# Performance work log

Measured on AMD Instinct MI355X. Metric: run time of the kernel, lower is better.

## Reference

```python
import jax, jax.numpy as jnp
import numpy as np

N_V, N_G, K, C_IN, DW, NB, E = 8192, 4096, 128, 128, 64, 4, 65536
SIGMA, CUT = 4.0, 8.0


def setup_inputs() -> dict:
    key = jax.random.key(0)
    ks = iter(jax.random.split(key, 64))
    s = 0.05
    def rn(shape):
        return jax.random.normal(next(ks), shape, dtype=jnp.float32) * s
    p = {}
    p['vertices'] = jax.random.uniform(next(ks), (N_V, 3), dtype=jnp.float32) * 30.0
    p['graph_pos'] = jax.random.uniform(next(ks), (N_G, 3), dtype=jnp.float32) * 30.0
    p['x_in'] = jax.random.normal(next(ks), (N_V, C_IN), dtype=jnp.float32)
    p['graph_x'] = jax.random.normal(next(ks), (N_G, C_IN), dtype=jnp.float32)
    p['mass'] = jax.random.uniform(next(ks), (N_V,), dtype=jnp.float32) + 0.5
    p['evals'] = jax.random.uniform(next(ks), (K,), dtype=jnp.float32) * 10.0
    p['evecs'] = jax.random.normal(next(ks), (N_V, K), dtype=jnp.float32) * 0.011
    p['gradX'] = jax.random.normal(next(ks), (N_V, N_V), dtype=jnp.float32) * 0.01
    p['gradY'] = jax.random.normal(next(ks), (N_V, N_V), dtype=jnp.float32) * 0.01
    p['graph_edge_index'] = jax.random.randint(next(ks), (2, E), 0, N_G)
    p['graph_edge_weight'] = jax.random.uniform(next(ks), (E,), dtype=jnp.float32)
    p['lin1_w'] = rn((C_IN, DW)); p['lin1_b'] = rn((DW,))
    p['lin2_w'] = rn((C_IN, DW)); p['lin2_b'] = rn((DW,))
    p['diff_time'] = jax.random.uniform(next(ks), (NB, DW), dtype=jnp.float32) * 0.5 + 0.01
    p['A_re'] = rn((NB, DW, DW)); p['A_im'] = rn((NB, DW, DW))
    p['mlp_w0'] = rn((NB, 3 * DW, DW)); p['mlp_b0'] = rn((NB, DW))
    p['mlp_w1'] = rn((NB, DW, DW)); p['mlp_b1'] = rn((NB, DW))
    p['mlp_w2'] = rn((NB, DW, DW)); p['mlp_b2'] = rn((NB, DW))
    p['gcn1_w'] = rn((NB, DW, DW)); p['gcn1_b'] = rn((NB, DW))
    p['gcn2_w'] = rn((NB, DW, DW)); p['gcn2_b'] = rn((NB, DW))
    p['gs_w'] = rn((NB, DW, DW)); p['gs_b'] = rn((NB, DW))
    p['sg_w'] = rn((NB, DW, DW)); p['sg_b'] = rn((NB, DW))
    return p


def _gcn_conv(x, src, dst, ew, W, b, n):
    # PyG GCNConv with self-loops (fill 1.0): D^-1/2 (A+I) D^-1/2 (x W) + b
    xw = x @ W
    deg = jnp.ones((n,), xw.dtype).at[dst].add(ew)
    dinv = 1.0 / jnp.sqrt(deg)
    norm = dinv[src] * ew * dinv[dst]
    agg = jnp.zeros_like(xw).at[dst].add(norm[:, None] * xw[src])
    return agg + xw / deg[:, None] + b


def _forward(vertices, graph_pos, x_in, graph_x, mass, evals, evecs, gradX, gradY,
             graph_edge_weight, lin1_w, lin1_b, lin2_w, lin2_b, diff_time, A_re, A_im,
             mlp_w0, mlp_b0, mlp_w1, mlp_b1, mlp_w2, mlp_b2,
             gcn1_w, gcn1_b, gcn2_w, gcn2_b, gs_w, gs_b, sg_w, sg_b, graph_edge_index):
    n_v = vertices.shape[0]
    # torch.cdist + cutoff + exp(-d/sigma), under no_grad in the original
    d = jnp.sqrt(jnp.maximum(jnp.sum((vertices[:, None, :] - graph_pos[None, :, :]) ** 2, -1), 0.0))
    Wb = jax.lax.stop_gradient(jnp.where(d < CUT, jnp.exp(-d / SIGMA), 0.0))  # [n_v, n_g]
    deg_v = 1.0 + Wb.sum(1)  # vertex in-degree incl. self-loop (graphsurf direction)
    deg_g = 1.0 + Wb.sum(0)  # graph-node in-degree incl. self-loop (surfgraph direction)
    rsv = 1.0 / jnp.sqrt(deg_v)
    rsg = 1.0 / jnp.sqrt(deg_g)
    src, dst = graph_edge_index[0], graph_edge_index[1]
    diff_x = x_in @ lin1_w + lin1_b
    gx = graph_x @ lin2_w + lin2_b
    n_g = gx.shape[0]
    for i in range(NB):
        # --- DiffusionNet block (spectral) ---
        t = jnp.maximum(diff_time[i], 1e-8)
        spec = evecs.T @ (diff_x * mass[:, None])              # [K, DW]
        xd = evecs @ (jnp.exp(-evals[:, None] * t[None, :]) * spec)
        gX = gradX @ xd                                         # real part of gradient
        gY = gradY @ xd                                         # imag part of gradient
        br = gX @ A_re[i] - gY @ A_im[i]
        bi = gY @ A_re[i] + gX @ A_im[i]
        gf = jnp.tanh(gX * br + gY * bi)                        # spatial gradient features
        h = jnp.concatenate([diff_x, xd, gf], axis=-1)
        h = jax.nn.relu(h @ mlp_w0[i] + mlp_b0[i])
        h = jax.nn.relu(h @ mlp_w1[i] + mlp_b1[i])
        diff_x = diff_x + h @ mlp_w2[i] + mlp_b2[i]
        # --- internal graph GCN (eval mode: dropout = identity) ---
        gx = jax.nn.relu(_gcn_conv(gx, src, dst, graph_edge_weight, gcn1_w[i], gcn1_b[i], n_g))
        gx = _gcn_conv(gx, src, dst, graph_edge_weight, gcn2_w[i], gcn2_b[i], n_g)
        # --- bipartite GCNConvs on concatenated nodes ---
        xall = jnp.concatenate([diff_x, gx], axis=0)
        xw = xall @ gs_w[i]   # graphsurf: graph -> surface edges
        os_v = xw[:n_v] / deg_v[:, None] + (Wb @ xw[n_v:]) * rsv[:, None] + gs_b[i]
        os_g = xw[n_v:] + gs_b[i]
        xw2 = xall @ sg_w[i]  # surfgraph: surface -> graph edges
        og_g = xw2[n_v:] / deg_g[:, None] + (Wb.T @ xw2[:n_v]) * rsg[:, None] + sg_b[i]
        og_v = xw2[:n_v] + sg_b[i]
        diff_x = 0.5 * (os_v + og_v)
        gx = 0.5 * (os_g + og_g)
    return diff_x  # [n_v, C_out]


def reference(vertices, graph_pos, x_in, graph_x, mass, evals, evecs, gradX, gradY,
              graph_edge_index, graph_edge_weight, lin1_w, lin1_b, lin2_w, lin2_b,
              diff_time, A_re, A_im, mlp_w0, mlp_b0, mlp_w1, mlp_b1, mlp_w2, mlp_b2,
              gcn1_w, gcn1_b, gcn2_w, gcn2_b, gs_w, gs_b, sg_w, sg_b):
    return _forward(vertices, graph_pos, x_in, graph_x, mass, evals, evecs, gradX, gradY,
                    graph_edge_weight, lin1_w, lin1_b, lin2_w, lin2_b, diff_time, A_re, A_im,
                    mlp_w0, mlp_b0, mlp_w1, mlp_b1, mlp_w2, mlp_b2,
                    gcn1_w, gcn1_b, gcn2_w, gcn2_b, gs_w, gs_b, sg_w, sg_b, graph_edge_index)
```

## Files before the change

### kernel.cpp

```cpp
#include <hip/hip_runtime.h>
#include <hip/hip_bf16.h>

typedef unsigned short u16;
typedef __attribute__((ext_vector_type(8))) short sh8;
typedef __attribute__((ext_vector_type(4))) float f32x4;

#define NV 8192
#define NG 4096
#define NE 65536

__device__ __forceinline__ u16 f2bf(float f) {
  __hip_bfloat16 h = __float2bfloat16(f);
  return __builtin_bit_cast(u16, h);
}

__device__ __forceinline__ void gl_lds16(const void* g, void* l) {
  __builtin_amdgcn_global_load_lds(
      (const __attribute__((address_space(1))) void*)g,
      (__attribute__((address_space(3))) void*)l, 16, 0, 0);
}

__global__ void k_fill4(float* __restrict__ deg_v, float* __restrict__ deg_g,
                        float* __restrict__ deg_e, int* __restrict__ cnt) {
  int i = blockIdx.x * 256 + threadIdx.x;
// ... 86 lines not shown

__global__ void k_edge_prep(const int* __restrict__ eidx, const float* __restrict__ ew,
                            float* __restrict__ deg_e, int* __restrict__ cnt) {
  int e = blockIdx.x * 256 + threadIdx.x;
  if (e < NE) { int d = eidx[NE + e]; atomicAdd(&deg_e[d], ew[e]); atomicAdd(&cnt[d], 1); }
}

__global__ __launch_bounds__(1024) void k_scan(const int* __restrict__ cnt,
    int* __restrict__ row_ptr, int* __restrict__ cursor) {
  __shared__ int buf0[1024], buf1[1024];
  int t = threadIdx.x;
  int b = t * 4;
  int c0 = cnt[b], c1 = cnt[b + 1], c2 = cnt[b + 2], c3 = cnt[b + 3];
  int s = c0 + c1 + c2 + c3;
  buf0[t] = s;
  __syncthreads();
  int* src = buf0; int* dst = buf1;
  for (int off = 1; off < 1024; off <<= 1) {
    int v = src[t];
    if (t >= off) v += src[t - off];
    dst[t] = v;
    __syncthreads();
    int* tmp = src; src = dst; dst = tmp;
  }
  int excl = (t == 0) ? 0 : src[t - 1];
  int r0 = excl, r1 = excl + c0, r2 = excl + c0 + c1, r3 = excl + c0 + c1 + c2;
  row_ptr[b] = r0; row_ptr[b + 1] = r1; row_ptr[b + 2] = r2; row_ptr[b + 3] = r3;
  cursor[b] = r0; cursor[b + 1] = r1; cursor[b + 2] = r2; cursor[b + 3] = r3;
  if (t == 1023) row_ptr[4096] = src[1023];
}

__global__ void k_scatter(const int* __restrict__ eidx, const float* __restrict__ ew,
                          const float* __restrict__ dinv, int* __restrict__ cursor,
                          int* __restrict__ csrc, float* __restrict__ cnorm) {
  int e = blockIdx.x * 256 + threadIdx.x;
  if (e < NE) {
    int s = eidx[e], d = eidx[NE + e];
    int slot = atomicAdd(&cursor[d], 1);
    csrc[slot] = s;
    cnorm[slot] = dinv[s] * ew[e] * dinv[d];
  }
}

__global__ __launch_bounds__(256) void k_evecsT(const float* __restrict__ ev, u16* __restrict__ evT) {
  __shared__ float tile[32][33];
  int t = threadIdx.x;
  int v0 = blockIdx.x * 32, k0 = blockIdx.y * 32;
  int r = t >> 3, c4 = (t & 7) * 4;
  float4 x = *(const float4*)(ev + (size_t)(v0 + r) * 128 + k0 + c4);
  tile[r][c4] = x.x; tile[r][c4 + 1] = x.y; tile[r][c4 + 2] = x.z; tile[r][c4 + 3] = x.w;
  __syncthreads();
  u16* dst = evT + (size_t)(k0 + r) * NV + v0 + c4;
  dst[0] = f2bf(tile[c4][r]); dst[1] = f2bf(tile[c4 + 1][r]);
  dst[2] = f2bf(tile[c4 + 2][r]); dst[3] = f2bf(tile[c4 + 3][r]);
}

__global__ __launch_bounds__(256) void gemm_setup3(
    const float* __restrict__ gXm, const float* __restrict__ gYm,
    const u16* __restrict__ evT, float* __restrict__ parts,
    int z, int kchunk) {
  extern __shared__ __align__(16) char smem[];
  const int t = threadIdx.x;
  const int lane = t & 63, wave = t >> 6;
  const int rl = lane & 15, hi = lane >> 4;
  int b = blockIdx.x;
  const int zi = b % z; b /= z;
  const int mb = b & 31;
  const int mat = b >> 5;
  const float* A = mat ? gYm : gXm;
  const int m0 = mb * 256;
  const int kbeg = zi * kchunk;
  const int nt = kchunk >> 5;
  const int wm = wave * 64;

  f32x4 acc[4][8];
  #pragma unroll
  for (int a = 0; a < 4; a++)
    #pragma unroll
    for (int bb = 0; bb < 8; bb++) acc[a][bb] = f32x4{0.f, 0.f, 0.f, 0.f};

  auto STAGE = [&](int buf, int k0) {
    char* aB = smem + buf * 40960;
    #pragma unroll
    for (int jj = 0; jj < 8; jj++) {
      int R0 = wave * 64 + jj * 8;
      int r = R0 + (lane >> 3);
      int s = lane & 7;
      gl_lds16(A + (size_t)(m0 + r) * NV + k0 + ((s ^ (r & 7)) << 2), aB + R0 * 128);
    }
    char* bB = smem + buf * 40960 + 32768;
    #pragma unroll
    for (int jj = 0; jj < 2; jj++) {
      int R0 = wave * 32 + jj * 16;
      int n = R0 + (lane >> 2);
      int s = lane & 3;
      gl_lds16(evT + (size_t)n * NV + k0 + ((s ^ ((n >> 1) & 3)) << 3), bB + R0 * 64);
    }
  };

  auto COMPUTE = [&](int buf) {
    const float* Af = (const float*)(smem + buf * 40960);
    const u16* Bf = (const u16*)(smem + buf * 40960 + 32768);
    sh8 av[4], bv[8];
    #pragma unroll
    for (int mf = 0; mf < 4; mf++) {
      int r = wm + mf * 16 + rl;
      f32x4 lo = *(const f32x4*)(Af + r * 32 + (((2 * hi) ^ (r & 7)) << 2));
      f32x4 h4 = *(const f32x4*)(Af + r * 32 + (((2 * hi + 1) ^ (r & 7)) << 2));
      sh8 v;
      v[0] = (short)f2bf(lo[0]); v[1] = (short)f2bf(lo[1]);
      v[2] = (short)f2bf(lo[2]); v[3] = (short)f2bf(lo[3]);
      v[4] = (short)f2bf(h4[0]); v[5] = (short)f2bf(h4[1]);
      v[6] = (short)f2bf(h4[2]); v[7] = (short)f2bf(h4[3]);
      av[mf] = v;
    }
    #pragma unroll
    for (int nf = 0; nf < 8; nf++) {
      int n = nf * 16 + rl;
      bv[nf] = *(const sh8*)(Bf + n * 32 + ((hi ^ ((n >> 1) & 3)) << 3));
    }
    #pragma unroll
    for (int mf = 0; mf < 4; mf++)
      #pragma unroll
      for (int nf = 0; nf < 8; nf++)
        acc[mf][nf] = __builtin_amdgcn_mfma_f32_16x16x32_bf16(av[mf], bv[nf], acc[mf][nf], 0, 0, 0);
  };

  STAGE(0, kbeg);
  if (nt > 1) STAGE(1, kbeg + 32);
  for (int ti = 0; ti < nt; ti++) {
    if (ti + 1 < nt) { asm volatile("s_waitcnt vmcnt(10)" ::: "memory"); }
    else             { asm volatile("s_waitcnt vmcnt(0)" ::: "memory"); }
    __builtin_amdgcn_sched_barrier(0);
    __builtin_amdgcn_s_barrier();
    COMPUTE(ti & 1);
    __builtin_amdgcn_sched_barrier(0);
    __builtin_amdgcn_s_barrier();
    if (ti + 2 < nt) STAGE(ti & 1, kbeg + (ti + 2) * 32);
  }

  float* C = parts + (size_t)(mat * z + zi) * (NV * 128);
  #pragma unroll
  for (int mf = 0; mf < 4; mf++)
    #pragma unroll
    for (int nf = 0; nf < 8; nf++) {
      int row = m0 + wm + mf * 16 + hi * 4;
      int col = nf * 16 + rl;
      #pragma unroll
      for (int q = 0; q < 4; q++)
        C[(size_t)(row + q) * 128 + col] = acc[mf][nf][q];
    }
}

__global__ __launch_bounds__(256) void gemm_panel2(
    const u16* __restrict__ WbP, const u16* __restrict__ WbTP,
    const u16* __restrict__ xwgT, const u16* __restrict__ xw2vT,
    float* __restrict__ parts) {
  __shared__ __align__(16) char smem[49152];
  const int t = threadIdx.x;
  const int lane = t & 63, wave = t >> 6;
  const int rl = lane & 15, hi = lane >> 4;
  int bid = blockIdx.x;
  const u16* Apan; const u16* BT; int KT, ldbt, mb, z;
  float* Cbase;
  if (bid < 512) {
    Apan = WbP; BT = xwgT; KT = 64; ldbt = NG;
    mb = bid >> 3; z = bid & 7;
    Cbase = parts + (size_t)z * NV * 64;
  } else {
    bid -= 512;
    Apan = WbTP; BT = xw2vT; KT = 128; ldbt = NV;
    mb = bid >> 4; z = bid & 15;
    Cbase = parts + (size_t)8 * NV * 64 + (size_t)z * NG * 64;
  }
  const int ktpz = 8;
  const int kt0 = z * ktpz;
  const int wm = wave * 32;

  f32x4 acc[2][4];
  #pragma unroll
  for (int a = 0; a < 2; a++)
    #pragma unroll
    for (int b = 0; b < 4; b++) acc[a][b] = f32x4{0.f, 0.f, 0.f, 0.f};

  auto STAGE = [&](int buf, int kt) {
    char* aB = smem + buf * 24576;
    const u16* tbase = Apan + ((size_t)mb * KT + kt) * 8192;
    #pragma unroll
    for (int jj = 0; jj < 4; jj++) {
      int j = wave * 4 + jj;
      gl_lds16(tbase + j * 512 + lane * 8, aB + j * 1024);
    }
    char* bB = aB + 16384;
    #pragma unroll
    for (int jj = 0; jj < 2; jj++) {
      int j = wave * 2 + jj;
      int n = 8 * j + (lane >> 3);
      const u16* srcb = BT + (size_t)n * ldbt + kt * 64 + (((lane & 7) ^ (n & 7)) << 3);
      gl_lds16(srcb, bB + j * 1024);
    }
  };

  auto COMPUTE = [&](int buf) {
    const u16* Af = (const u16*)(smem + buf * 24576);
    const u16* Bf = Af + 8192;
    #pragma unroll
    for (int step = 0; step < 2; step++) {
      sh8 av[2], bv[4];
      int s = step * 4 + hi;
      #pragma unroll
      for (int mf = 0; mf < 2; mf++) {
        int r = wm + mf * 16 + rl;
        av[mf] = *(const sh8*)(Af + r * 64 + ((s ^ (r & 7)) << 3));
      }
      #pragma unroll
      for (int nf = 0; nf < 4; nf++) {
        int n = nf * 16 + rl;
        bv[nf] = *(const sh8*)(Bf + n * 64 + ((s ^ (n & 7)) << 3));
      }
      #pragma unroll
      for (int mf = 0; mf < 2; mf++)
        #pragma unroll
        for (int nf = 0; nf < 4; nf++)
          acc[mf][nf] = __builtin_amdgcn_mfma_f32_16x16x32_bf16(av[mf], bv[nf], acc[mf][nf], 0, 0, 0);
    }
  };

  STAGE(0, kt0);
  STAGE(1, kt0 + 1);
  for (int ti = 0; ti < ktpz; ti++) {
    if (ti + 1 < ktpz) { asm volatile("s_waitcnt vmcnt(6)" ::: "memory"); }
    else               { asm volatile("s_waitcnt vmcnt(0)" ::: "memory"); }
    __builtin_amdgcn_sched_barrier(0);
    __builtin_amdgcn_s_barrier();
    COMPUTE(ti & 1);
    __builtin_amdgcn_sched_barrier(0);
    __builtin_amdgcn_s_barrier();
    if (ti + 2 < ktpz) STAGE(ti & 1, kt0 + ti + 2);
  }

  #pragma unroll
  for (int mf = 0; mf < 2; mf++)
    #pragma unroll
    for (int nf = 0; nf < 4; nf++) {
      int row = mb * 128 + wm + mf * 16 + hi * 4;
      int col = nf * 16 + rl;
      #pragma unroll
      for (int q = 0; q < 4; q++)
        Cbase[(size_t)(row + q) * 64 + col] = acc[mf][nf][q];
    }
}

__global__ void k_reduce_combine(const float* __restrict__ parts,
    const float* __restrict__ xw_v, const float* __restrict__ xw2_v,
    const float* __restrict__ xw_g, const float* __restrict__ xw2_g,
    const float* __restrict__ inv_deg_v, const float* __restrict__ rsv,
    const float* __restrict__ inv_deg_g, const float* __restrict__ rsg,
    const float* __restrict__ gsb, const float* __restrict__ sgb,
    float* __restrict__ dx, float* __restrict__ gx) {
  int idx = blockIdx.x * 256 + threadIdx.x;
  if (idx < NV * 64) {
    float s = parts[idx];
    #pragma unroll
    for (int z = 1; z < 8; z++) s += parts[(size_t)z * NV * 64 + idx];
    int v = idx >> 6, c = idx & 63;
    dx[idx] = 0.5f * (xw_v[idx] * inv_deg_v[v] + s * rsv[v] + gsb[c] + xw2_v[idx] + sgb[c]);
  } else {
    int j = idx - NV * 64;
    const float* src = parts + (size_t)8 * NV * 64;
    float s = src[j];
    #pragma unroll
    for (int z = 1; z < 16; z++) s += src[(size_t)z * NG * 64 + j];
    int g = j >> 6, c = j & 63;
    gx[j] = 0.5f * (xw_g[j] + gsb[c] + xw2_g[j] * inv_deg_g[g] + s * rsg[g] + sgb[c]);
  }
}

__global__ __launch_bounds__(256) void gemm_bf16(
    const u16* __restrict__ Ab, int lda, const u16* __restrict__ BT, int ldbt,
    float* __restrict__ parts, int M, int kchunk) {
  __shared__ __align__(16) char smem[49152];
  const int t = threadIdx.x;
  const int lane = t & 63, wave = t >> 6;
  const int m0 = blockIdx.x * 128;
  const int kbeg = blockIdx.z * kchunk;
  const int nt = kchunk >> 6;
  const int wm = (wave >> 1) * 64, wn = (wave & 1) * 32;
  const int arl = lane >> 3, asl = lane & 7;

  f32x4 acc[4][2];
  #pragma unroll
  for (int a = 0; a < 4; a++)
    #pragma unroll
    for (int b = 0; b < 2; b++) acc[a][b] = f32x4{0.f, 0.f, 0.f, 0.f};

  auto STAGE = [&](int buf, int k0) {
    char* base = smem + buf * 24576;
    #pragma unroll
    for (int j = 0; j < 4; j++) {
      int R0 = (wave * 4 + j) * 8;
      int r = R0 + arl;
      int gs = asl ^ (r & 7);
      gl_lds16(Ab + (size_t)(m0 + r) * lda + k0 + gs * 8, base + R0 * 128);
    }
    char* bb = base + 16384;
    #pragma unroll
    for (int j = 0; j < 2; j++) {
      int R0 = (wave * 2 + j) * 8;
      int r = R0 + arl;
      int gs = asl ^ (r & 7);
      gl_lds16(BT + (size_t)r * ldbt + k0 + gs * 8, bb + R0 * 128);
    }
  };

  auto COMPUTE = [&](int buf) {
    char* base = smem + buf * 24576;
    const u16* Af = (const u16*)base;
    const u16* Bf = (const u16*)(base + 16384);
    #pragma unroll
    for (int kk = 0; kk < 2; kk++) {
      sh8 av[4], bv[2];
      #pragma unroll
      for (int mf = 0; mf < 4; mf++) {
        int r = wm + mf * 16 + (lane & 15);
        int g = kk * 4 + (lane >> 4);
        av[mf] = *(const sh8*)(Af + r * 64 + (g ^ (r & 7)) * 8);
      }
      #pragma unroll
      for (int nf = 0; nf < 2; nf++) {
        int r = wn + nf * 16 + (lane & 15);
        int g = kk * 4 + (lane >> 4);
        bv[nf] = *(const sh8*)(Bf + r * 64 + (g ^ (r & 7)) * 8);
      }
      #pragma unroll
      for (int mf = 0; mf < 4; mf++)
        #pragma unroll
        for (int nf = 0; nf < 2; nf++)
          acc[mf][nf] = __builtin_amdgcn_mfma_f32_16x16x32_bf16(av[mf], bv[nf], acc[mf][nf], 0, 0, 0);
    }
  };

  STAGE(0, kbeg);
  if (nt > 1) STAGE(1, kbeg + 64);
  for (int ti = 0; ti < nt; ti++) {
    if (ti + 1 < nt) { asm volatile("s_waitcnt vmcnt(6)" ::: "memory"); }
    else             { asm volatile("s_waitcnt vmcnt(0)" ::: "memory"); }
    __builtin_amdgcn_sched_barrier(0);
    __builtin_amdgcn_s_barrier();
    COMPUTE(ti & 1);
    __builtin_amdgcn_sched_barrier(0);
    __builtin_amdgcn_s_barrier();
// ... 168 lines not shown
    }
  } else {
    float* lW = (float*)shm;
    int rb = bid - 128;
    for (int i = t; i < 4096; i += 256) lW[i] = W[i];
    __syncthreads();
    int row = rb * 4 + (t >> 6), c = t & 63;
    const float* Ar = gxb + (size_t)row * 64;
    float acc = 0.f;
    #pragma unroll 8
    for (int k = 0; k < 64; k++) acc += Ar[k] * lW[k * 64 + c];
    xw1[(size_t)row * 64 + c] = acc;
  }
}

__global__ __launch_bounds__(256) void k_specagg(
    const u16* __restrict__ evT, const u16* __restrict__ mdxT,
    float* __restrict__ parts,
    const float* __restrict__ xw, const int* __restrict__ rp,
    const int* __restrict__ csrc, const float* __restrict__ cnorm,
    const float* __restrict__ invdeg, const float* __restrict__ b1,
    const float* __restrict__ W2, float* __restrict__ out) {
  __shared__ __align__(16) char smem[49152];
  const int t = threadIdx.x;
  if (blockIdx.x < 64) {
    const int lane = t & 63, wave = t >> 6;
    const int kbeg = blockIdx.x * 128;
    const int wm = (wave >> 1) * 64, wn = (wave & 1) * 32;
    const int arl = lane >> 3, asl = lane & 7;
    f32x4 acc[4][2];
    #pragma unroll
    for (int a = 0; a < 4; a++)
      #pragma unroll
      for (int b = 0; b < 2; b++) acc[a][b] = f32x4{0.f, 0.f, 0.f, 0.f};
    auto STAGE = [&](int buf, int k0) {
      char* base = smem + buf * 24576;
      #pragma unroll
      for (int j = 0; j < 4; j++) {
        int R0 = (wave * 4 + j) * 8;
        int r = R0 + arl;
        int gs = asl ^ (r & 7);
        gl_lds16(evT + (size_t)r * NV + k0 + gs * 8, base + R0 * 128);
      }
      char* bb = base + 16384;
      #pragma unroll
      for (int j = 0; j < 2; j++) {
        int R0 = (wave * 2 + j) * 8;
        int r = R0 + arl;
        int gs = asl ^ (r & 7);
        gl_lds16(mdxT + (size_t)r * NV + k0 + gs * 8, bb + R0 * 128);
      }
    };
    auto COMPUTE = [&](int buf) {
      char* base = smem + buf * 24576;
      const u16* Af = (const u16*)base;
      const u16* Bf = (const u16*)(base + 16384);
      #pragma unroll
      for (int kk = 0; kk < 2; kk++) {
        sh8 av[4], bv[2];
        #pragma unroll
        for (int mf = 0; mf < 4; mf++) {
          int r = wm + mf * 16 + (lane & 15);
          int g = kk * 4 + (lane >> 4);
          av[mf] = *(const sh8*)(Af + r * 64 + (g ^ (r & 7)) * 8);
        }
        #pragma unroll
        for (int nf = 0; nf < 2; nf++) {
          int r = wn + nf * 16 + (lane & 15);
          int g = kk * 4 + (lane >> 4);
          bv[nf] = *(const sh8*)(Bf + r * 64 + (g ^ (r & 7)) * 8);
        }
        #pragma unroll
        for (int mf = 0; mf < 4; mf++)
          #pragma unroll
          for (int nf = 0; nf < 2; nf++)
            acc[mf][nf] = __builtin_amdgcn_mfma_f32_16x16x32_bf16(av[mf], bv[nf], acc[mf][nf], 0, 0, 0);
      }
    };
    STAGE(0, kbeg);
    STAGE(1, kbeg + 64);
    for (int ti = 0; ti < 2; ti++) {
      if (ti == 0) { asm volatile("s_waitcnt vmcnt(6)" ::: "memory"); }
      else         { asm volatile("s_waitcnt vmcnt(0)" ::: "memory"); }
      __builtin_amdgcn_sched_barrier(0);
      __builtin_amdgcn_s_barrier();
      COMPUTE(ti);
      __builtin_amdgcn_sched_barrier(0);
      __builtin_amdgcn_s_barrier();
    }
    float* C = parts + (size_t)blockIdx.x * 8192;
    const int lane2 = t & 63;
    #pragma unroll
    for (int mf = 0; mf < 4; mf++)
      #pragma unroll
      for (int nf = 0; nf < 2; nf++) {
        int row = wm + mf * 16 + (lane2 >> 4) * 4;
        int col = wn + nf * 16 + (lane2 & 15);
        #pragma unroll
        for (int q = 0; q < 4; q++)
          C[(size_t)(row + q) * 64 + col] = acc[mf][nf][q];
      }
  } else {
    float* lrow = (float*)smem;
    int g = (blockIdx.x - 64) * 4 + (t >> 6), c = t & 63;
    float acc = xw[(size_t)g * 64 + c] * invdeg[g] + b1[c];
    int j1 = rp[g + 1];
    for (int j = rp[g]; j < j1; j++) acc += cnorm[j] * xw[(size_t)csrc[j] * 64 + c];
    acc = fmaxf(acc, 0.f);
    lrow[t] = acc;
    __syncthreads();
    int grp = t & 192;
    float o = 0.f;
    #pragma unroll 8
    for (int k = 0; k < 64; k++) o += lrow[grp + k] * W2[k * 64 + c];
    out[(size_t)g * 64 + c] = o;
  }
}

__global__ __launch_bounds__(256) void k_redagg(
    const float* __restrict__ parts, const float* __restrict__ evals,
    const float* __restrict__ dt, float* __restrict__ Es,
    const float* __restrict__ xw, const int* __restrict__ rp,
    const int* __restrict__ csrc, const float* __restrict__ cnorm,
    const float* __restrict__ invdeg, const float* __restrict__ b2,
    const float* __restrict__ gsw, const float* __restrict__ sgw,
    float* __restrict__ xw_g, float* __restrict__ xw2_g, u16* __restrict__ xwgT) {
  __shared__ float lrow[256];
  int t = threadIdx.x;
  if (blockIdx.x < 32) {
    int i = blockIdx.x * 256 + t;
    float s = 0.f;
    #pragma unroll 8
    for (int z = 0; z < 64; z++) s += parts[(size_t)z * 8192 + i];
    int k = i >> 6, c = i & 63;
    Es[i] = expf(-evals[k] * fmaxf(dt[c], 1e-8f)) * s;
  } else {
    int g = (blockIdx.x - 32) * 4 + (t >> 6), c = t & 63;
    float acc = xw[(size_t)g * 64 + c] * invdeg[g] + b2[c];
    int j1 = rp[g + 1];
    for (int j = rp[g]; j < j1; j++) acc += cnorm[j] * xw[(size_t)csrc[j] * 64 + c];
    lrow[t] = acc;
    __syncthreads();
    int grp = t & 192;
    float p = 0.f, q = 0.f;
    #pragma unroll 8
    for (int k = 0; k < 64; k++) {
      float r = lrow[grp + k];
      p += r * gsw[k * 64 + c];
      q += r * sgw[k * 64 + c];
    }
    xw_g[(size_t)g * 64 + c] = p;
    xw2_g[(size_t)g * 64 + c] = q;
    xwgT[(size_t)c * NG + g] = f2bf(p);
  }
}

__global__ __launch_bounds__(256) void k_xdgf(const float* __restrict__ evecs,
    const float* __restrict__ GXE, const float* __restrict__ GYE,
    const float* __restrict__ Es, const float* __restrict__ Are,
    const float* __restrict__ Aim, float* __restrict__ xd, float* __restrict__ gf) {
  __shared__ float lE[8192];
  __shared__ float lr[4096], li[4096];
  __shared__ float lgx[256], lgy[256];
  int t = threadIdx.x;
  for (int i = t; i < 8192; i += 256) lE[i] = Es[i];
  for (int i = t; i < 4096; i += 256) { lr[i] = Are[i]; li[i] = Aim[i]; }
  __syncthreads();
  int wr = t >> 6, c = t & 63;
  #pragma unroll
  for (int rg = 0; rg < 2; rg++) {
    int row = blockIdx.x * 8 + rg * 4 + wr;
    const float* er = evecs + (size_t)row * 128;
    const float* xr = GXE + (size_t)row * 128;
    const float* yr = GYE + (size_t)row * 128;
    float a0 = 0, a1 = 0, a2 = 0;
    #pragma unroll 8
    for (int k = 0; k < 128; k++) {
      float s = lE[k * 64 + c];
      a0 += er[k] * s; a1 += xr[k] * s; a2 += yr[k] * s;
    }
    lgx[wr * 64 + c] = a1;
    lgy[wr * 64 + c] = a2;
    __syncthreads();
    float br = 0.f, bi = 0.f;
    #pragma unroll 8
    for (int k = 0; k < 64; k++) {
      float gx = lgx[wr * 64 + k], gy = lgy[wr * 64 + k];
      float ar = lr[k * 64 + c], ai = li[k * 64 + c];
      br += gx * ar - gy * ai;
      bi += gy * ar + gx * ai;
    }
    xd[(size_t)row * 64 + c] = a0;
    gf[(size_t)row * 64 + c] = tanhf(a1 * br + a2 * bi);
    __syncthreads();
  }
}

__global__ __launch_bounds__(256) void k_mlp0(const float* __restrict__ dx,
    const float* __restrict__ xd, const float* __restrict__ gf,
    const float* __restrict__ W0, const float* __restrict__ b0, float* __restrict__ h1) {
  __shared__ float lW[12288];
  __shared__ float lb[64];
  int t = threadIdx.x;
  for (int i = t; i < 12288; i += 256) lW[i] = W0[i];
  if (t < 64) lb[t] = b0[t];
  __syncthreads();
  int wr = t >> 6, c = t & 63;
  #pragma unroll
  for (int rg = 0; rg < 2; rg++) {
    int row = blockIdx.x * 8 + rg * 4 + wr;
    const float* a0 = dx + (size_t)row * 64;
    const float* a1 = xd + (size_t)row * 64;
    const float* a2 = gf + (size_t)row * 64;
    float acc = lb[c];
    #pragma unroll 8
    for (int k = 0; k < 64; k++) acc += a0[k] * lW[k * 64 + c];
    #pragma unroll 8
    for (int k = 0; k < 64; k++) acc += a1[k] * lW[(64 + k) * 64 + c];
    #pragma unroll 8
    for (int k = 0; k < 64; k++) acc += a2[k] * lW[(128 + k) * 64 + c];
    h1[(size_t)row * 64 + c] = fmaxf(acc, 0.f);
  }
}

__global__ __launch_bounds__(256) void k_mlp12_dual(const float* __restrict__ h1,
    const float* __restrict__ W1, const float* __restrict__ b1,
    const float* __restrict__ W2, const float* __restrict__ b2,
    const float* __restrict__ dx, const float* __restrict__ gsw,
    const float* __restrict__ sgw, float* __restrict__ xw_v,
    float* __restrict__ xw2_v, u16* __restrict__ xw2vT) {
  __shared__ float l1[4096], l2[4096], lg[4096], ls[4096];
  __shared__ float lb1[64], lb2[64], lrow[256], lrow2[256];
  int t = threadIdx.x;
  for (int i = t; i < 4096; i += 256) {
    l1[i] = W1[i]; l2[i] = W2[i]; lg[i] = gsw[i]; ls[i] = sgw[i];
  }
  if (t < 64) lb1[t] = b1[t];
  else if (t < 128) lb2[t - 64] = b2[t - 64];
  __syncthreads();
  int wr = t >> 6, c = t & 63;
  #pragma unroll
  for (int rg = 0; rg < 2; rg++) {
    int row = blockIdx.x * 8 + rg * 4 + wr;
    const float* hr = h1 + (size_t)row * 64;
    float h2 = lb1[c];
    #pragma unroll 8
    for (int k = 0; k < 64; k++) h2 += hr[k] * l1[k * 64 + c];
    h2 = fmaxf(h2, 0.f);
    lrow[wr * 64 + c] = h2;
    __syncthreads();
    float o = lb2[c] + dx[(size_t)row * 64 + c];
    #pragma unroll 8
    for (int k = 0; k < 64; k++) o += lrow[wr * 64 + k] * l2[k * 64 + c];
    lrow2[wr * 64 + c] = o;
    __syncthreads();
    float p = 0.f, q = 0.f;
    #pragma unroll 8
    for (int k = 0; k < 64; k++) {
      float a = lrow2[wr * 64 + k];
      p += a * lg[k * 64 + c];
      q += a * ls[k * 64 + c];
    }
    xw_v[(size_t)row * 64 + c] = p;
    xw2_v[(size_t)row * 64 + c] = q;
    xw2vT[(size_t)c * NV + row] = f2bf(q);
    __syncthreads();
  }
}

__global__ void k_combine(const float* __restrict__ xw_v, const float* __restrict__ Wbp,
    const float* __restrict__ xw2_v, const float* __restrict__ xw_g,
    const float* __restrict__ WbTp, const float* __restrict__ xw2_g,
    const float* __restrict__ inv_deg_v, const float* __restrict__ rsv,
    const float* __restrict__ inv_deg_g, const float* __restrict__ rsg,
    const float* __restrict__ gsb, const float* __restrict__ sgb,
    float* __restrict__ dx, float* __restrict__ gx) {
  int idx = blockIdx.x * 256 + threadIdx.x;
  if (idx < NV * 64) {
    int v = idx >> 6, c = idx & 63;
    dx[idx] = 0.5f * (xw_v[idx] * inv_deg_v[v] + Wbp[idx] * rsv[v] + gsb[c] + xw2_v[idx] + sgb[c]);
  } else {
    int j = idx - NV * 64;
    int g = j >> 6, c = j & 63;
    gx[j] = 0.5f * (xw_g[j] + gsb[c] + xw2_g[j] * inv_deg_g[g] + WbTp[j] * rsg[g] + sgb[c]);
  }
}

extern "C" void kernel_launch(void* const* d_in, const int* in_sizes, int n_in,
                              void* d_out, int out_size, void* d_ws, size_t ws_size,
                              hipStream_t stream) {
  const float* vertices  = (const float*)d_in[0];
  const float* graph_pos = (const float*)d_in[1];
  const float* x_in      = (const float*)d_in[2];
  const float* graph_x   = (const float*)d_in[3];
  const float* mass      = (const float*)d_in[4];
  const float* evals     = (const float*)d_in[5];
  const float* evecs     = (const float*)d_in[6];
  const float* gradX     = (const float*)d_in[7];
  const float* gradY     = (const float*)d_in[8];
  const int*   eidx      = (const int*)d_in[9];
  const float* ew        = (const float*)d_in[10];
  const float* lin1_w    = (const float*)d_in[11];
  const float* lin1_b    = (const float*)d_in[12];
  const float* lin2_w    = (const float*)d_in[13];
  const float* lin2_b    = (const float*)d_in[14];
  const float* diff_time = (const float*)d_in[15];
  const float* A_re      = (const float*)d_in[16];
  const float* A_im      = (const float*)d_in[17];
  const float* mlp_w0    = (const float*)d_in[18];
  const float* mlp_b0    = (const float*)d_in[19];
  const float* mlp_w1    = (const float*)d_in[20];
  const float* mlp_b1    = (const float*)d_in[21];
  const float* mlp_w2    = (const float*)d_in[22];
  const float* mlp_b2    = (const float*)d_in[23];
  const float* gcn1_w    = (const float*)d_in[24];
  const float* gcn1_b    = (const float*)d_in[25];
  const float* gcn2_w    = (const float*)d_in[26];
  const float* gcn2_b    = (const float*)d_in[27];
  const float* gs_w      = (const float*)d_in[28];
  const float* gs_b      = (const float*)d_in[29];
  const float* sg_w      = (const float*)d_in[30];
  const float* sg_b      = (const float*)d_in[31];

  char* base = (char*)d_ws;
  size_t off = 0;
  auto alloc = [&](size_t nbytes) -> void* {
    void* p = base + off;
    off += (nbytes + 255) & ~(size_t)255;
    return p;
  };
  const size_t MBy = 1024 * 1024;
  u16*   evecsT  = (u16*)alloc((size_t)128 * NV * 2);
  float* GXE2    = (float*)alloc((size_t)2 * NV * 128 * 4);
  float* GXE     = GXE2;
  float* GYE     = GXE2 + (size_t)NV * 128;
  u16*   mdxT    = (u16*)alloc((size_t)64 * NV * 2);
  float* Es      = (float*)alloc(8192 * 4);
  float* diffx   = (float*)alloc((size_t)NV * 64 * 4);
  float* gxb     = (float*)alloc((size_t)NG * 64 * 4);
  float* xd      = (float*)alloc((size_t)NV * 64 * 4);
  float* gf      = (float*)alloc((size_t)NV * 64 * 4);
  float* h1      = (float*)alloc((size_t)NV * 64 * 4);
  float* xw_v    = (float*)alloc((size_t)NV * 64 * 4);
  float* xw2_v   = (float*)alloc((size_t)NV * 64 * 4);
  float* xw_g    = (float*)alloc((size_t)NG * 64 * 4);
  float* xw2_g   = (float*)alloc((size_t)NG * 64 * 4);
  float* xw1     = (float*)alloc((size_t)NG * 64 * 4);
  float* xw2k    = (float*)alloc((size_t)NG * 64 * 4);
  u16*   xwgT    = (u16*)alloc((size_t)64 * NG * 2);
  u16*   xw2vT   = (u16*)alloc((size_t)64 * NV * 2);
  float* Wbp     = (float*)alloc((size_t)NV * 64 * 4);
  float* WbTp    = (float*)alloc((size_t)NG * 64 * 4);
  float* deg_v   = (float*)alloc(NV * 4);
  float* inv_deg_v = (float*)alloc(NV * 4);
  float* rsv     = (float*)alloc(NV * 4);
  float* deg_g   = (float*)alloc(NG * 4);
  float* inv_deg_g = (float*)alloc(NG * 4);
  float* rsg     = (float*)alloc(NG * 4);
  float* deg_e   = (float*)alloc(NG * 4);
  float* invdeg_e = (float*)alloc(NG * 4);
  float* dinv_e  = (float*)alloc(NG * 4);
  int*   cnt     = (int*)alloc(NG * 4);
  int*   row_ptr = (int*)alloc((NG + 1) * 4);
  int*   cursor  = (int*)alloc(NG * 4);
  int*   csr_src = (int*)alloc(NE * 4);
  float* csr_norm = (float*)alloc(NE * 4);

  size_t avail = ws_size > off ? ws_size - off : 0;
  u16 *WbP = nullptr, *WbTP = nullptr, *WbRow = nullptr;
  float* parts;
  int zsu;
  if (avail >= 162 * MBy) {
    WbP  = (u16*)alloc((size_t)NV * NG * 2);
    WbTP = (u16*)alloc((size_t)NG * NV * 2);
    parts = (float*)alloc(32 * MBy);
    zsu = 4;
  } else if (avail >= 97 * MBy) {
    WbRow = (u16*)alloc((size_t)NV * NG * 2);
    parts = (float*)alloc(32 * MBy);
    zsu = 4;
  } else {
    WbRow = (u16*)alloc((size_t)NV * NG * 2);
    parts = (float*)alloc(16 * MBy);
    zsu = 2;
  }
  if (off > ws_size) return;

  dim3 B256(256);

  k_fill4<<<dim3(80), B256, 0, stream>>>(deg_v, deg_g, deg_e, cnt);
  k_wb_build<<<dim3(128, 64), B256, 0, stream>>>(vertices, graph_pos, WbRow, WbP, WbTP, deg_v, deg_g);
  k_edge_prep<<<dim3(256), B256, 0, stream>>>(eidx, ew, deg_e, cnt);
  k_recips<<<dim3(64), B256, 0, stream>>>(deg_v, inv_deg_v, rsv, deg_g, inv_deg_g, rsg,
                                          deg_e, invdeg_e, dinv_e);
  k_scan<<<dim3(1), dim3(1024), 0, stream>>>(cnt, row_ptr, cursor);
  k_scatter<<<dim3(256), B256, 0, stream>>>(eidx, ew, dinv_e, cursor, csr_src, csr_norm);
  k_evecsT<<<dim3(256, 4), B256, 0, stream>>>(evecs, evecsT);
  gemm_setup3<<<dim3(2 * 32 * zsu), B256, 81920, stream>>>(
      gradX, gradY, evecsT, parts, zsu, 8192 / zsu);
  k_reduce2<<<dim3(2048), B256, 0, stream>>>(parts, GXE2, NV * 128, zsu);
  k_lin_both<<<dim3(3072), B256, 0, stream>>>(x_in, graph_x, lin1_w, lin1_b, lin2_w, lin2_b, diffx, gxb);

  for (int i = 0; i < 4; i++) {
    const float* dtrow = diff_time + i * 64;
    k_front<<<dim3(128 + 1024), B256, 0, stream>>>(diffx, mass, mdxT, gxb,
        gcn1_w + i * 4096, xw1);
    k_specagg<<<dim3(64 + 1024), B256, 0, stream>>>(evecsT, mdxT, parts,
        xw1, row_ptr, csr_src, csr_norm, invdeg_e, gcn1_b + i * 64,
        gcn2_w + i * 4096, xw2k);
    k_redagg<<<dim3(32 + 1024), B256, 0, stream>>>(parts, evals, dtrow, Es,
        xw2k, row_ptr, csr_src, csr_norm, invdeg_e, gcn2_b + i * 64,
        gs_w + i * 4096, sg_w + i * 4096, xw_g, xw2_g, xwgT);
    k_xdgf<<<dim3(1024), B256, 0, stream>>>(evecs, GXE, GYE, Es, A_re + i * 4096, A_im + i * 4096, xd, gf);
    k_mlp0<<<dim3(1024), B256, 0, stream>>>(diffx, xd, gf, mlp_w0 + i * 12288, mlp_b0 + i * 64, h1);
    k_mlp12_dual<<<dim3(1024), B256, 0, stream>>>(h1, mlp_w1 + i * 4096, mlp_b1 + i * 64,
        mlp_w2 + i * 4096, mlp_b2 + i * 64, diffx, gs_w + i * 4096, sg_w + i * 4096,
        xw_v, xw2_v, xw2vT);
    if (WbP != nullptr) {
      gemm_panel2<<<dim3(1024), B256, 0, stream>>>(WbP, WbTP, xwgT, xw2vT, parts);
      k_reduce_combine<<<dim3(3072), B256, 0, stream>>>(parts, xw_v, xw2_v, xw_g, xw2_g,
          inv_deg_v, rsv, inv_deg_g, rsg, gs_b + i * 64, sg_b + i * 64, diffx, gxb);
    } else {
      gemm_bf16<<<dim3(64, 1, 8), B256, 0, stream>>>(WbRow, NG, xwgT, NG, parts, NV, 512);
      k_reduce<<<dim3(512), B256, 0, stream>>>(parts, Wbp, NV * 64, 8);
      gemm_k<64, false, true><<<dim3(32, 1, 16), B256, 0, stream>>>(
          WbRow, nullptr, 1 << 30, xw2vT, parts, NG, 64, NG, NV, 512);
      k_reduce<<<dim3(256), B256, 0, stream>>>(parts, WbTp, NG * 64, 16);
      k_combine<<<dim3(3072), B256, 0, stream>>>(xw_v, Wbp, xw2_v, xw_g, WbTp, xw2_g,
          inv_deg_v, rsv, inv_deg_g, rsg, gs_b + i * 64, sg_b + i * 64, diffx, gxb);
    }
  }

  hipMemcpyAsync(d_out, diffx, (size_t)NV * 64 * 4, hipMemcpyDeviceToDevice, stream);
}
```

Baseline: 925.7 us.

## Overlap Wb panel GEMM with xdgf by merging into one launch

Splits the combined Wb/WbT panel GEMM. The Wb @ xw_g half depends only on the graph branch, so it now runs as extra blocks inside the xdgf kernel launch, while the WbT half runs after the MLP kernels as its own kernel. This lets the memory-heavy panel GEMM share the GPU with the VALU-bound xdgf work and moves part of the panel work off the critical path. The merged kernel uses a larger 66KB shared-memory footprint for all blocks, which may reduce occupancy of the xdgf blocks.

Result: no change. 934.1 us (+0.9%).

```diff
diff --git a/kernel.cpp b/kernel.cpp
--- a/kernel.cpp
+++ b/kernel.cpp
@@ -262,27 +262,150 @@
     }
 }
 
-__global__ __launch_bounds__(256) void gemm_panel2(
-    const u16* __restrict__ WbP, const u16* __restrict__ WbTP,
-    const u16* __restrict__ xwgT, const u16* __restrict__ xw2vT,
+__global__ __launch_bounds__(256) void k_xdgf_wbp(
+    const float* __restrict__ evecs, const float* __restrict__ GXE,
+    const float* __restrict__ GYE, const float* __restrict__ Es,
+    const float* __restrict__ Are, const float* __restrict__ Aim,
+    float* __restrict__ xd, float* __restrict__ gf,
+    const u16* __restrict__ WbP, const u16* __restrict__ xwgT,
+    float* __restrict__ parts) {
+  __shared__ __align__(16) char shm[67584];
+  const int t = threadIdx.x;
+  if (blockIdx.x < 1024) {
+    float* lE  = (float*)shm;
+    float* lr  = lE + 8192;
+    float* li  = lr + 4096;
+    float* lgx = li + 4096;
+    float* lgy = lgx + 256;
+    for (int i = t; i < 8192; i += 256) lE[i] = Es[i];
+    for (int i = t; i < 4096; i += 256) { lr[i] = Are[i]; li[i] = Aim[i]; }
+    __syncthreads();
+    int wr = t >> 6, c = t & 63;
+    #pragma unroll
+    for (int rg = 0; rg < 2; rg++) {
+      int row = blockIdx.x * 8 + rg * 4 + wr;
+      const float* er = evecs + (size_t)row * 128;
+      const float* xr = GXE + (size_t)row * 128;
+      const float* yr = GYE + (size_t)row * 128;
+      float a0 = 0, a1 = 0, a2 = 0;
+      #pragma unroll 8
+      for (int k = 0; k < 128; k++) {
+        float s = lE[k * 64 + c];
+        a0 += er[k] * s; a1 += xr[k] * s; a2 += yr[k] * s;
+      }
+      lgx[wr * 64 + c] = a1;
+      lgy[wr * 64 + c] = a2;
+      __syncthreads();
+      float br = 0.f, bi = 0.f;
+      #pragma unroll 8
+      for (int k = 0; k < 64; k++) {
+        float gx = lgx[wr * 64 + k], gy = lgy[wr * 64 + k];
+        float ar = lr[k * 64 + c], ai = li[k * 64 + c];
+        br += gx * ar - gy * ai;
+        bi += gy * ar + gx * ai;
+      }
+      xd[(size_t)row * 64 + c] = a0;
+      gf[(size_t)row * 64 + c] = tanhf(a1 * br + a2 * bi);
+      __syncthreads();
+    }
+  } else {
+    char* smem = shm;
+    const int lane = t & 63, wave = t >> 6;
+    const int rl = lane & 15, hi = lane >> 4;
+    int bid = blockIdx.x - 1024;
+    const int mb = bid >> 3, z = bid & 7;
+    const int KT = 64;
+    float* Cbase = parts + (size_t)z * NV * 64;
+    const int ktpz = 8;
+    const int kt0 = z * ktpz;
+    const int wm = wave * 32;
+
+    f32x4 acc[2][4];
+    #pragma unroll
+    for (int a = 0; a < 2; a++)
+      #pragma unroll
+      for (int b = 0; b < 4; b++) acc[a][b] = f32x4{0.f, 0.f, 0.f, 0.f};
+
+    auto STAGE = [&](int buf, int kt) {
+      char* aB = smem + buf * 24576;
+      const u16* tbase = WbP + ((size_t)mb * KT + kt) * 8192;
+      #pragma unroll
+      for (int jj = 0; jj < 4; jj++) {
+        int j = wave * 4 + jj;
+        gl_lds16(tbase + j * 512 + lane * 8, aB + j * 1024);
+      }
+      char* bB = aB + 16384;
+      #pragma unroll
+      for (int jj = 0; jj < 2; jj++) {
+        int j = wave * 2 + jj;
+        int n = 8 * j + (lane >> 3);
+        const u16* srcb = xwgT + (size_t)n * NG + kt * 64 + (((lane & 7) ^ (n & 7)) << 3);
+        gl_lds16(srcb, bB + j * 1024);
+      }
+    };
+
+    auto COMPUTE = [&](int buf) {
+      const u16* Af = (const u16*)(smem + buf * 24576);
+      const u16* Bf = Af + 8192;
+      #pragma unroll
+      for (int step = 0; step < 2; step++) {
+        sh8 av[2], bv[4];
+        int s = step * 4 + hi;
+        #pragma unroll
+        for (int mf = 0; mf < 2; mf++) {
+          int r = wm + mf * 16 + rl;
+          av[mf] = *(const sh8*)(Af + r * 64 + ((s ^ (r & 7)) << 3));
+        }
+        #pragma unroll
+        for (int nf = 0; nf < 4; nf++) {
+          int n = nf * 16 + rl;
+          bv[nf] = *(const sh8*)(Bf + n * 64 + ((s ^ (n & 7)) << 3));
+        }
+        #pragma unroll
+        for (int mf = 0; mf < 2; mf++)
+          #pragma unroll
+          for (int nf = 0; nf < 4; nf++)
+            acc[mf][nf] = __builtin_amdgcn_mfma_f32_16x16x32_bf16(av[mf], bv[nf], acc[mf][nf], 0, 0, 0);
+      }
+    };
+
+    STAGE(0, kt0);
+    STAGE(1, kt0 + 1);
+    for (int ti = 0; ti < ktpz; ti++) {
+      if (ti + 1 < ktpz) { asm volatile("s_waitcnt vmcnt(6)" ::: "memory"); }
+      else               { asm volatile("s_waitcnt vmcnt(0)" ::: "memory"); }
+      __builtin_amdgcn_sched_barrier(0);
+      __builtin_amdgcn_s_barrier();
+      COMPUTE(ti & 1);
+      __builtin_amdgcn_sched_barrier(0);
+      __builtin_amdgcn_s_barrier();
+      if (ti + 2 < ktpz) STAGE(ti & 1, kt0 + ti + 2);
+    }
+
+    #pragma unroll
+    for (int mf = 0; mf < 2; mf++)
+      #pragma unroll
+      for (int nf = 0; nf < 4; nf++) {
+        int row = mb * 128 + wm + mf * 16 + hi * 4;
+        int col = nf * 16 + rl;
+        #pragma unroll
+        for (int q = 0; q < 4; q++)
+          Cbase[(size_t)(row + q) * 64 + col] = acc[mf][nf][q];
+      }
+  }
+}
+
+__global__ __launch_bounds__(256) void k_panelT(
+    const u16* __restrict__ WbTP, const u16* __restrict__ xw2vT,
     float* __restrict__ parts) {
   __shared__ __align__(16) char smem[49152];
   const int t = threadIdx.x;
   const int lane = t & 63, wave = t >> 6;
   const int rl = lane & 15, hi = lane >> 4;
   int bid = blockIdx.x;
-  const u16* Apan; const u16* BT; int KT, ldbt, mb, z;
-  float* Cbase;
-  if (bid < 512) {
-    Apan = WbP; BT = xwgT; KT = 64; ldbt = NG;
-    mb = bid >> 3; z = bid & 7;
-    Cbase = parts + (size_t)z * NV * 64;
-  } else {
-    bid -= 512;
-    Apan = WbTP; BT = xw2vT; KT = 128; ldbt = NV;
-    mb = bid >> 4; z = bid & 15;
-    Cbase = parts + (size_t)8 * NV * 64 + (size_t)z * NG * 64;
-  }
+  const int mb = bid >> 4, z = bid & 15;
+  const int KT = 128;
+  float* Cbase = parts + (size_t)8 * NV * 64 + (size_t)z * NG * 64;
   const int ktpz = 8;
   const int kt0 = z * ktpz;
   const int wm = wave * 32;
@@ -295,7 +418,7 @@
 
   auto STAGE = [&](int buf, int kt) {
     char* aB = smem + buf * 24576;
-    const u16* tbase = Apan + ((size_t)mb * KT + kt) * 8192;
+    const u16* tbase = WbTP + ((size_t)mb * KT + kt) * 8192;
     #pragma unroll
     for (int jj = 0; jj < 4; jj++) {
       int j = wave * 4 + jj;
@@ -306,7 +429,7 @@
     for (int jj = 0; jj < 2; jj++) {
       int j = wave * 2 + jj;
       int n = 8 * j + (lane >> 3);
-      const u16* srcb = BT + (size_t)n * ldbt + kt * 64 + (((lane & 7) ^ (n & 7)) << 3);
+      const u16* srcb = xw2vT + (size_t)n * NV + kt * 64 + (((lane & 7) ^ (n & 7)) << 3);
       gl_lds16(srcb, bB + j * 1024);
     }
   };
@@ -781,47 +904,6 @@
     xw_g[(size_t)g * 64 + c] = p;
     xw2_g[(size_t)g * 64 + c] = q;
     xwgT[(size_t)c * NG + g] = f2bf(p);
-  }
-}
-
-__global__ __launch_bounds__(256) void k_xdgf(const float* __restrict__ evecs,
-    const float* __restrict__ GXE, const float* __restrict__ GYE,
-    const float* __restrict__ Es, const float* __restrict__ Are,
-    const float* __restrict__ Aim, float* __restrict__ xd, float* __restrict__ gf) {
-  __shared__ float lE[8192];
-  __shared__ float lr[4096], li[4096];
-  __shared__ float lgx[256], lgy[256];
-  int t = threadIdx.x;
-  for (int i = t; i < 8192; i += 256) lE[i] = Es[i];
-  for (int i = t; i < 4096; i += 256) { lr[i] = Are[i]; li[i] = Aim[i]; }
-  __syncthreads();
-  int wr = t >> 6, c = t & 63;
-  #pragma unroll
-  for (int rg = 0; rg < 2; rg++) {
-    int row = blockIdx.x * 8 + rg * 4 + wr;
-    const float* er = evecs + (size_t)row * 128;
-    const float* xr = GXE + (size_t)row * 128;
-    const float* yr = GYE + (size_t)row * 128;
-    float a0 = 0, a1 = 0, a2 = 0;
-    #pragma unroll 8
-    for (int k = 0; k < 128; k++) {
-      float s = lE[k * 64 + c];
-      a0 += er[k] * s; a1 += xr[k] * s; a2 += yr[k] * s;
-    }
-    lgx[wr * 64 + c] = a1;
-    lgy[wr * 64 + c] = a2;
-    __syncthreads();
-    float br = 0.f, bi = 0.f;
-    #pragma unroll 8
-    for (int k = 0; k < 64; k++) {
-      float gx = lgx[wr * 64 + k], gy = lgy[wr * 64 + k];
-      float ar = lr[k * 64 + c], ai = li[k * 64 + c];
-      br += gx * ar - gy * ai;
-      bi += gy * ar + gx * ai;
-    }
-    xd[(size_t)row * 64 + c] = a0;
-    gf[(size_t)row * 64 + c] = tanhf(a1 * br + a2 * bi);
-    __syncthreads();
   }
 }
 
@@ -893,6 +975,47 @@
     xw_v[(size_t)row * 64 + c] = p;
     xw2_v[(size_t)row * 64 + c] = q;
     xw2vT[(size_t)c * NV + row] = f2bf(q);
+    __syncthreads();
+  }
+}
+
+__global__ __launch_bounds__(256) void k_xdgf(const float* __restrict__ evecs,
+    const float* __restrict__ GXE, const float* __restrict__ GYE,
+    const float* __restrict__ Es, const float* __restrict__ Are,
+    const float* __restrict__ Aim, float* __restrict__ xd, float* __restrict__ gf) {
+  __shared__ float lE[8192];
+  __shared__ float lr[4096], li[4096];
+  __shared__ float lgx[256], lgy[256];
+  int t = threadIdx.x;
+  for (int i = t; i < 8192; i += 256) lE[i] = Es[i];
+  for (int i = t; i < 4096; i += 256) { lr[i] = Are[i]; li[i] = Aim[i]; }
+  __syncthreads();
+  int wr = t >> 6, c = t & 63;
+  #pragma unroll
+  for (int rg = 0; rg < 2; rg++) {
+    int row = blockIdx.x * 8 + rg * 4 + wr;
+    const float* er = evecs + (size_t)row * 128;
+    const float* xr = GXE + (size_t)row * 128;
+    const float* yr = GYE + (size_t)row * 128;
+    float a0 = 0, a1 = 0, a2 = 0;
+    #pragma unroll 8
+    for (int k = 0; k < 128; k++) {
+      float s = lE[k * 64 + c];
+      a0 += er[k] * s; a1 += xr[k] * s; a2 += yr[k] * s;
+    }
+    lgx[wr * 64 + c] = a1;
+    lgy[wr * 64 + c] = a2;
+    __syncthreads();
+    float br = 0.f, bi = 0.f;
+    #pragma unroll 8
+    for (int k = 0; k < 64; k++) {
+      float gx = lgx[wr * 64 + k], gy = lgy[wr * 64 + k];
+      float ar = lr[k * 64 + c], ai = li[k * 64 + c];
+      br += gx * ar - gy * ai;
+      bi += gy * ar + gx * ai;
+    }
+    xd[(size_t)row * 64 + c] = a0;
+    gf[(size_t)row * 64 + c] = tanhf(a1 * br + a2 * bi);
     __syncthreads();
   }
 }
@@ -1040,16 +1163,22 @@
     k_redagg<<<dim3(32 + 1024), B256, 0, stream>>>(parts, evals, dtrow, Es,
         xw2k, row_ptr, csr_src, csr_norm, invdeg_e, gcn2_b + i * 64,
         gs_w + i * 4096, sg_w + i * 4096, xw_g, xw2_g, xwgT);
-    k_xdgf<<<dim3(1024), B256, 0, stream>>>(evecs, GXE, GYE, Es, A_re + i * 4096, A_im + i * 4096, xd, gf);
-    k_mlp0<<<dim3(1024), B256, 0, stream>>>(diffx, xd, gf, mlp_w0 + i * 12288, mlp_b0 + i * 64, h1);
-    k_mlp12_dual<<<dim3(1024), B256, 0, stream>>>(h1, mlp_w1 + i * 4096, mlp_b1 + i * 64,
-        mlp_w2 + i * 4096, mlp_b2 + i * 64, diffx, gs_w + i * 4096, sg_w + i * 4096,
-        xw_v, xw2_v, xw2vT);
     if (WbP != nullptr) {
-      gemm_panel2<<<dim3(1024), B256, 0, stream>>>(WbP, WbTP, xwgT, xw2vT, parts);
+      k_xdgf_wbp<<<dim3(1024 + 512), B256, 0, stream>>>(evecs, GXE, GYE, Es,
+          A_re + i * 4096, A_im + i * 4096, xd, gf, WbP, xwgT, parts);
+      k_mlp0<<<dim3(1024), B256, 0, stream>>>(diffx, xd, gf, mlp_w0 + i * 12288, mlp_b0 + i * 64, h1);
+      k_mlp12_dual<<<dim3(1024), B256, 0, stream>>>(h1, mlp_w1 + i * 4096, mlp_b1 + i * 64,
+          mlp_w2 + i * 4096, mlp_b2 + i * 64, diffx, gs_w + i * 4096, sg_w + i * 4096,
+          xw_v, xw2_v, xw2vT);
+      k_panelT<<<dim3(512), B256, 0, stream>>>(WbTP, xw2vT, parts);
       k_reduce_combine<<<dim3(3072), B256, 0, stream>>>(parts, xw_v, xw2_v, xw_g, xw2_g,
           inv_deg_v, rsv, inv_deg_g, rsg, gs_b + i * 64, sg_b + i * 64, diffx, gxb);
     } else {
+      k_xdgf<<<dim3(1024), B256, 0, stream>>>(evecs, GXE, GYE, Es, A_re + i * 4096, A_im + i * 4096, xd, gf);
+      k_mlp0<<<dim3(1024), B256, 0, stream>>>(diffx, xd, gf, mlp_w0 + i * 12288, mlp_b0 + i * 64, h1);
+      k_mlp12_dual<<<dim3(1024), B256, 0, stream>>>(h1, mlp_w1 + i * 4096, mlp_b1 + i * 64,
+          mlp_w2 + i * 4096, mlp_b2 + i * 64, diffx, gs_w + i * 4096, sg_w + i * 4096,
+          xw_v, xw2_v, xw2vT);
       gemm_bf16<<<dim3(64, 1, 8), B256, 0, stream>>>(WbRow, NG, xwgT, NG, parts, NV, 512);
       k_reduce<<<dim3(512), B256, 0, stream>>>(parts, Wbp, NV * 64, 8);
       gemm_k<64, false, true><<<dim3(32, 1, 16), B256, 0, stream>>>(
```
